# Performance work log

Measured on AMD Instinct MI355X. Metric: run time of the kernel, lower is better.

## Reference

```python
import jax, jax.numpy as jnp
import numpy as np

N = 12288      # num_nodes
D = 128        # seg_emb
NUM_GRAPHS = 48
NUM_CLS = 27   # classes 24,25,26 are excluded by the module


def setup_inputs() -> dict:
    key = jax.random.key(0)
    k1, k2, k3, k4 = jax.random.split(key, 4)
    z1 = jax.random.normal(k1, (N, D), dtype=jnp.float32)
    z2 = jax.random.normal(k2, (N, D), dtype=jnp.float32)
    cls_label = jax.random.randint(k3, (N,), 0, NUM_CLS, dtype=jnp.int32)
    batch = jnp.sort(jax.random.randint(k4, (N,), 0, NUM_GRAPHS, dtype=jnp.int32))
    return {"z1": z1, "z2": z2, "cls_label": cls_label, "batch": batch}


def reference(z1, z2, cls_label, batch):
    # Pairwise validity mask: same graph AND same class AND class not in {24,25,26}.
    # This reproduces the nested gather->matmul->scatter loops: each (graph, class)
    # block of z1 @ z2.T is kept, everything else stays zero. Single-node classes
    # (skipped in the original) only contribute a diagonal entry, which is zeroed.
    same_graph = batch[:, None] == batch[None, :]            # [N, N]
    same_cls = cls_label[:, None] == cls_label[None, :]      # [N, N]
    excluded = (cls_label >= 24) & (cls_label <= 26)         # [N]
    mask = same_graph & same_cls & ~excluded[:, None]

    scores = jnp.matmul(z1, z2.T)                            # [N, N] inner products
    out = jnp.where(mask, scores, jnp.float32(0.0))
    n = out.shape[0]
    idx = jnp.arange(n)
    out = out.at[idx, idx].set(0.0)                          # zero the diagonal
    return out
```

## Files before the change

kernel.cpp:

```cpp
#include <hip/hip_runtime.h>

#define NN 12288
#define DD 128

__global__ __launch_bounds__(256) void segdec_kernel(
    const float* __restrict__ z1, const float* __restrict__ z2,
    const int* __restrict__ cls, const int* __restrict__ batch,
    float* __restrict__ out)
{
    const int i   = blockIdx.x;
    const int tid = threadIdx.x;
    __shared__ float z1s[DD];

    if (tid < DD / 4) {
        reinterpret_cast<float4*>(z1s)[tid] =
            reinterpret_cast<const float4*>(z1 + (size_t)i * DD)[tid];
    }

    const float4 zero4 = make_float4(0.f, 0.f, 0.f, 0.f);
    float4* __restrict__ orow = reinterpret_cast<float4*>(out + (size_t)i * NN);
    #pragma unroll
    for (int k = 0; k < (NN / 4) / 256; ++k) {
        orow[tid + k * 256] = zero4;
    }

    const int batch_i = batch[i];
    const int cls_i   = cls[i];

    __syncthreads();

    if (cls_i >= 24) return;

    int lo, hi;
    {
        int l = 0, r = NN;
        while (l < r) { int m = (l + r) >> 1; if (batch[m] < batch_i) l = m + 1; else r = m; }
        lo = l;
        r = NN;
        while (l < r) { int m = (l + r) >> 1; if (batch[m] <= batch_i) l = m + 1; else r = m; }
        hi = l;
    }

    for (int j = lo + tid; j < hi; j += 256) {
        if (j != i && cls[j] == cls_i) {
            const float4* __restrict__ zrow =
                reinterpret_cast<const float4*>(z2 + (size_t)j * DD);
            float s = 0.f;
            #pragma unroll
            for (int k = 0; k < DD / 4; ++k) {
                const float4 a = reinterpret_cast<const float4*>(z1s)[k];
                const float4 b = zrow[k];
                s = fmaf(a.x, b.x, s);
                s = fmaf(a.y, b.y, s);
                s = fmaf(a.z, b.z, s);
                s = fmaf(a.w, b.w, s);
            }
            out[(size_t)i * NN + j] = s;
        }
    }
}

extern "C" void kernel_launch(void* const* d_in, const int* in_sizes, int n_in,
                              void* d_out, int out_size, void* d_ws, size_t ws_size,
                              hipStream_t stream) {
    const float* z1    = (const float*)d_in[0];
    const float* z2    = (const float*)d_in[1];
    const int*   cls   = (const int*)d_in[2];
    const int*   batch = (const int*)d_in[3];
    float*       out   = (float*)d_out;

    segdec_kernel<<<NN, 256, 0, stream>>>(z1, z2, cls, batch, out);
}
```

Measured before the change: 699.0 us.

## Split zero-fill into separate kernel and assign one wavefront per output row

Moves zeroing of the full N×N output into a dedicated grid-stride kernel, then launches a sparse kernel where each 64-lane wavefront handles one row, so a 256-thread block covers four rows and stages four z1 rows in shared memory. This frees the per-row dot-product work from the full-row zero store and matches the lane count to the typical per-graph segment size. It costs an extra launch and a second pass that rewrites the few nonzero entries after zeroing.

Result: faster. 673.0 us (-3.7%).

```diff
diff --git a/kernel.cpp b/kernel.cpp
--- a/kernel.cpp
+++ b/kernel.cpp
@@ -3,53 +3,58 @@
 #define NN 12288
 #define DD 128
 
-__global__ __launch_bounds__(256) void segdec_kernel(
+__global__ __launch_bounds__(256) void zero_fill(float4* __restrict__ out) {
+    const size_t total  = (size_t)NN * NN / 4;
+    const size_t stride = (size_t)gridDim.x * blockDim.x;
+    const float4 z = make_float4(0.f, 0.f, 0.f, 0.f);
+    for (size_t idx = (size_t)blockIdx.x * blockDim.x + threadIdx.x;
+         idx < total; idx += stride) {
+        out[idx] = z;
+    }
+}
+
+__global__ __launch_bounds__(256) void sparse_fill(
     const float* __restrict__ z1, const float* __restrict__ z2,
     const int* __restrict__ cls, const int* __restrict__ batch,
     float* __restrict__ out)
 {
-    const int i   = blockIdx.x;
-    const int tid = threadIdx.x;
-    __shared__ float z1s[DD];
+    const int wave = threadIdx.x >> 6;
+    const int lane = threadIdx.x & 63;
+    const int i    = blockIdx.x * 4 + wave;
 
-    if (tid < DD / 4) {
-        reinterpret_cast<float4*>(z1s)[tid] =
-            reinterpret_cast<const float4*>(z1 + (size_t)i * DD)[tid];
+    __shared__ float z1s[4][DD];
+    {
+        const float2* src =
+            reinterpret_cast<const float2*>(z1 + (size_t)blockIdx.x * 4 * DD);
+        reinterpret_cast<float2*>(&z1s[0][0])[threadIdx.x] = src[threadIdx.x];
     }
-
-    const float4 zero4 = make_float4(0.f, 0.f, 0.f, 0.f);
-    float4* __restrict__ orow = reinterpret_cast<float4*>(out + (size_t)i * NN);
-    #pragma unroll
-    for (int k = 0; k < (NN / 4) / 256; ++k) {
-        orow[tid + k * 256] = zero4;
-    }
-
-    const int batch_i = batch[i];
-    const int cls_i   = cls[i];
-
     __syncthreads();
 
+    const int cls_i = cls[i];
     if (cls_i >= 24) return;
+    const int batch_i = batch[i];
 
     int lo, hi;
     {
         int l = 0, r = NN;
-        while (l < r) { int m = (l + r) >> 1; if (batch[m] < batch_i) l = m + 1; else r = m; }
+        while (l < r) { int m = (l + r) >> 1; if (batch[m] <  batch_i) l = m + 1; else r = m; }
         lo = l;
         r = NN;
         while (l < r) { int m = (l + r) >> 1; if (batch[m] <= batch_i) l = m + 1; else r = m; }
         hi = l;
     }
 
-    for (int j = lo + tid; j < hi; j += 256) {
+    for (int j = lo + lane; j < hi; j += 64) {
         if (j != i && cls[j] == cls_i) {
-            const float4* __restrict__ zrow =
+            const float4* __restrict__ zb =
                 reinterpret_cast<const float4*>(z2 + (size_t)j * DD);
+            const float4* __restrict__ za =
+                reinterpret_cast<const float4*>(&z1s[wave][0]);
             float s = 0.f;
             #pragma unroll
             for (int k = 0; k < DD / 4; ++k) {
-                const float4 a = reinterpret_cast<const float4*>(z1s)[k];
-                const float4 b = zrow[k];
+                const float4 a = za[k];
+                const float4 b = zb[k];
                 s = fmaf(a.x, b.x, s);
                 s = fmaf(a.y, b.y, s);
                 s = fmaf(a.z, b.z, s);
@@ -69,5 +74,6 @@
     const int*   batch = (const int*)d_in[3];
     float*       out   = (float*)d_out;
 
-    segdec_kernel<<<NN, 256, 0, stream>>>(z1, z2, cls, batch, out);
+    zero_fill<<<1024, 256, 0, stream>>>(reinterpret_cast<float4*>(out));
+    sparse_fill<<<NN / 4, 256, 0, stream>>>(z1, z2, cls, batch, out);
 }
```

## Fuse zero-fill and masked dot products into a single write per output

Applied to the files above, without the earlier changes.

Each output element is now written exactly once. A thread computes the masked dot products for its own float4 slot and stores the result, instead of first zero-filling the whole row and then scattering scalar stores over it. The shared-memory staging of the z1 row and its barrier are removed, so z1 is read directly from global memory or cache. The cost is that each thread handles up to four dot products serially, so work within the graph segment is spread unevenly across threads, and there is one extra warp-divergent branch.

New measurement: 666.4 us. 4.7% less time.

```diff
diff --git a/kernel.cpp b/kernel.cpp
--- a/kernel.cpp
+++ b/kernel.cpp
@@ -3,60 +3,64 @@
 #define NN 12288
 #define DD 128
 
-__global__ __launch_bounds__(256) void segdec_kernel(
+__global__ __launch_bounds__(256) void segdec_fused(
     const float* __restrict__ z1, const float* __restrict__ z2,
     const int* __restrict__ cls, const int* __restrict__ batch,
     float* __restrict__ out)
 {
     const int i   = blockIdx.x;
     const int tid = threadIdx.x;
-    __shared__ float z1s[DD];
+    float4* __restrict__ orow = reinterpret_cast<float4*>(out + (size_t)i * NN);
+    const float4 zero4 = make_float4(0.f, 0.f, 0.f, 0.f);
 
-    if (tid < DD / 4) {
-        reinterpret_cast<float4*>(z1s)[tid] =
-            reinterpret_cast<const float4*>(z1 + (size_t)i * DD)[tid];
-    }
-
-    const float4 zero4 = make_float4(0.f, 0.f, 0.f, 0.f);
-    float4* __restrict__ orow = reinterpret_cast<float4*>(out + (size_t)i * NN);
-    #pragma unroll
-    for (int k = 0; k < (NN / 4) / 256; ++k) {
-        orow[tid + k * 256] = zero4;
+    const int cls_i = cls[i];
+    if (cls_i >= 24) {
+        #pragma unroll
+        for (int k = 0; k < 12; ++k) orow[tid + k * 256] = zero4;
+        return;
     }
 
     const int batch_i = batch[i];
-    const int cls_i   = cls[i];
-
-    __syncthreads();
-
-    if (cls_i >= 24) return;
-
     int lo, hi;
     {
         int l = 0, r = NN;
-        while (l < r) { int m = (l + r) >> 1; if (batch[m] < batch_i) l = m + 1; else r = m; }
+        while (l < r) { int m = (l + r) >> 1; if (batch[m] <  batch_i) l = m + 1; else r = m; }
         lo = l;
         r = NN;
         while (l < r) { int m = (l + r) >> 1; if (batch[m] <= batch_i) l = m + 1; else r = m; }
         hi = l;
     }
 
-    for (int j = lo + tid; j < hi; j += 256) {
-        if (j != i && cls[j] == cls_i) {
-            const float4* __restrict__ zrow =
-                reinterpret_cast<const float4*>(z2 + (size_t)j * DD);
-            float s = 0.f;
+    const float4* __restrict__ za = reinterpret_cast<const float4*>(z1 + (size_t)i * DD);
+
+    for (int k = 0; k < 12; ++k) {
+        const int f4 = tid + k * 256;
+        const int c0 = f4 * 4;
+        float4 v = zero4;
+        if (c0 < hi && c0 + 4 > lo) {
+            float vv[4] = {0.f, 0.f, 0.f, 0.f};
             #pragma unroll
-            for (int k = 0; k < DD / 4; ++k) {
-                const float4 a = reinterpret_cast<const float4*>(z1s)[k];
-                const float4 b = zrow[k];
-                s = fmaf(a.x, b.x, s);
-                s = fmaf(a.y, b.y, s);
-                s = fmaf(a.z, b.z, s);
-                s = fmaf(a.w, b.w, s);
+            for (int u = 0; u < 4; ++u) {
+                const int j = c0 + u;
+                if (j >= lo && j < hi && j != i && cls[j] == cls_i) {
+                    const float4* __restrict__ zb =
+                        reinterpret_cast<const float4*>(z2 + (size_t)j * DD);
+                    float s = 0.f;
+                    #pragma unroll
+                    for (int d = 0; d < DD / 4; ++d) {
+                        const float4 a = za[d];
+                        const float4 b = zb[d];
+                        s = fmaf(a.x, b.x, s);
+                        s = fmaf(a.y, b.y, s);
+                        s = fmaf(a.z, b.z, s);
+                        s = fmaf(a.w, b.w, s);
+                    }
+                    vv[u] = s;
+                }
             }
-            out[(size_t)i * NN + j] = s;
+            v = make_float4(vv[0], vv[1], vv[2], vv[3]);
         }
+        orow[f4] = v;
     }
 }
 
@@ -69,5 +73,5 @@
     const int*   batch = (const int*)d_in[3];
     float*       out   = (float*)d_out;
 
-    segdec_kernel<<<NN, 256, 0, stream>>>(z1, z2, cls, batch, out);
+    segdec_fused<<<NN, 256, 0, stream>>>(z1, z2, cls, batch, out);
 }
```
